# Kernel optimization log

Measured on AMD Instinct MI355X. Metric: run time of the kernel, lower is better.

The kernel has to match this reference:

```python
import jax, jax.numpy as jnp
import numpy as np
import math

B, S, D, H = 4, 2048, 1024, 16
DK = D // H

def setup_inputs() -> dict:
    key = jax.random.key(0)
    ks = jax.random.split(key, 11)
    mk = lambda k, shape: jax.random.normal(k, shape, dtype=jnp.float32)
    inp = {
        'query': mk(ks[0], (B, S, D)),
        'key':   mk(ks[1], (B, S, D)),
        'value': mk(ks[2], (B, S, D)),
        'Wq': mk(ks[3], (D, D)) * 0.02, 'bq': jnp.zeros((D,), jnp.float32),
        'Wk': mk(ks[4], (D, D)) * 0.02, 'bk': jnp.zeros((D,), jnp.float32),
        'Wv': mk(ks[5], (D, D)) * 0.02, 'bv': jnp.zeros((D,), jnp.float32),
        'Wo': mk(ks[6], (D, D)) * 0.02, 'bo': jnp.zeros((D,), jnp.float32),
    }
    return inp

def reference(query, key, value, Wq, bq, Wk, bk, Wv, bv, Wo, bo):
    b, s, d = query.shape
    scale = 1.0 / math.sqrt(DK)
    def proj(x, W, bias):
        # nn.Linear: x @ W.T + b, then split heads -> [b, h, s, dk]
        return (x @ W.T + bias).reshape(b, s, H, DK).transpose(0, 2, 1, 3)
    q = proj(query, Wq, bq)
    k = proj(key, Wk, bk)
    v = proj(value, Wv, bv)
    scores = jnp.einsum('bhqd,bhkd->bhqk', q, k) * scale  # [b,h,s,s]
    attn = jax.nn.softmax(scores, axis=-1)
    # dropout is identity in eval/reference mode
    x = jnp.einsum('bhqk,bhkd->bhqd', attn, v)
    x = x.transpose(0, 2, 1, 3).reshape(b, s, d)
    return x @ Wo.T + bo
```

## Files before the change

kernel.cpp:

```cpp
#include <hip/hip_runtime.h>
#include <stdint.h>

#define DEV static __device__ __forceinline__

typedef __bf16 bf16_t;
typedef bf16_t bf16x8 __attribute__((ext_vector_type(8)));
typedef bf16_t bf16x4 __attribute__((ext_vector_type(4)));
typedef float f32x4 __attribute__((ext_vector_type(4)));

static constexpr int Bc = 4, Sc = 2048, Dc = 1024, Hc = 16, DKc = 64;
static constexpr int Mrows = Bc * Sc;

DEV unsigned short f2bf(float f) {
  unsigned int u = __float_as_uint(f);
  u += 0x7fffu + ((u >> 16) & 1u);
  return (unsigned short)(u >> 16);
}

DEV float fexp2(float x) {
#if __has_builtin(__builtin_amdgcn_exp2f)
  return __builtin_amdgcn_exp2f(x);
#else
  return exp2f(x);
#endif
}

#if __has_builtin(__builtin_amdgcn_mfma_f32_16x16x16_bf16)
DEV f32x4 mfma16(bf16x4 a, bf16x4 b, f32x4 c) {
  return __builtin_amdgcn_mfma_f32_16x16x16_bf16(a, b, c, 0, 0, 0);
}
#elif __has_builtin(__builtin_amdgcn_mfma_f32_16x16x16bf16_1k)
typedef short s16x4 __attribute__((ext_vector_type(4)));
DEV f32x4 mfma16(bf16x4 a, bf16x4 b, f32x4 c) {
  union U { bf16x4 h; s16x4 s; };
  U ua, ub; ua.h = a; ub.h = b;
  return __builtin_amdgcn_mfma_f32_16x16x16bf16_1k(ua.s, ub.s, c, 0, 0, 0);
}
#else
DEV f32x4 mfma16(bf16x4 a, bf16x4 b, f32x4 c) {
  asm("v_mfma_f32_16x16x16_bf16 %0, %1, %2, %0" : "+v"(c) : "v"(a), "v"(b));
  return c;
}
#endif

DEV void gload_lds16(const void* g, void* l) {
  __builtin_amdgcn_global_load_lds(
      (const __attribute__((address_space(1))) void*)g,
      (__attribute__((address_space(3))) void*)l, 16, 0, 0);
}

DEV bf16x8 cvt8(float4 a, float4 b) {
  bf16x8 r;
  r[0] = (bf16_t)a.x; r[1] = (bf16_t)a.y; r[2] = (bf16_t)a.z; r[3] = (bf16_t)a.w;
  r[4] = (bf16_t)b.x; r[5] = (bf16_t)b.y; r[6] = (bf16_t)b.z; r[7] = (bf16_t)b.w;
  return r;
}

__global__ void __launch_bounds__(256) cvt_bf16_seg_kernel(
    const float* __restrict__ s0, const float* __restrict__ s1,
    const float* __restrict__ s2, const float* __restrict__ s3,
    unsigned short* __restrict__ out, int lg) {
  int i = blockIdx.x * blockDim.x + threadIdx.x;
  int seg = i >> lg, j = i & ((1 << lg) - 1);
  const float* src = seg == 0 ? s0 : seg == 1 ? s1 : seg == 2 ? s2 : s3;
  float4 v = reinterpret_cast<const float4*>(src)[j];
  ushort4 o;
  o.x = f2bf(v.x); o.y = f2bf(v.y); o.z = f2bf(v.z); o.w = f2bf(v.w);
  reinterpret_cast<ushort4*>(out)[i] = o;
}

template <bool QKV>
__global__ void __launch_bounds__(256) gemm_dbuf_kernel(
    const void* __restrict__ A0v, const void* __restrict__ A1v,
    const void* __restrict__ A2v,
    const unsigned short* __restrict__ W0, const unsigned short* __restrict__ W1,
    const unsigned short* __restrict__ W2,
    const float* __restrict__ b0, const float* __restrict__ b1,
    const float* __restrict__ b2,
    void* __restrict__ C0, void* __restrict__ C1, void* __restrict__ C2,
    int M, int N, int K, float scale0) {
  __shared__ unsigned short lA[2][128 * 32];
  __shared__ unsigned short lB[2][128 * 32];
  const int t = threadIdx.x;
  const int wv = t >> 6, ln = t & 63;
  const int l15 = ln & 15, lhi = ln >> 4;

  const void* Av; const unsigned short* W;
  const float* bias; void* Cout; float scale; int mode;
  if (QKV) {
    const int z = blockIdx.z;
    Av = z == 0 ? A0v : z == 1 ? A1v : A2v;
    W = z == 0 ? W0 : z == 1 ? W1 : W2;
    bias = z == 0 ? b0 : z == 1 ? b1 : b2;
    Cout = z == 0 ? C0 : z == 1 ? C1 : C2;
    scale = z == 0 ? scale0 : 1.0f;
    mode = z == 2 ? 2 : 1;
  } else {
    Av = A0v; W = W0; bias = b0; Cout = C0; scale = scale0; mode = 0;
  }

  const int nwg = gridDim.x * gridDim.y;
  const int hw = blockIdx.y * gridDim.x + blockIdx.x;
  const int chunk = nwg >> 3;
  const int swzid = (hw & 7) * chunk + (hw >> 3);
  const int m0 = (swzid / gridDim.x) * 128, n0 = (swzid % gridDim.x) * 128;
  const int wr = wv >> 1, wc = wv & 1;
  const int swzR = (l15 & 3) << 4;

  const int rowA = t >> 2;
  const int colS = ((t & 3) ^ (rowA & 3)) * 8;
  const unsigned short* wS = W + (size_t)(n0 + rowA) * K + colS;
  const size_t rstep = (size_t)64 * K;
  const int d0 = t * 16, d1 = 4096 + t * 16;
  const float* aF = QKV ? (const float*)Av + (size_t)(m0 + rowA) * K + colS : nullptr;
  const unsigned short* aB =
      QKV ? nullptr : (const unsigned short*)Av + (size_t)(m0 + rowA) * K + colS;

  f32x4 acc[4][4] = {};

#define WSTAGE(bi, k0_)                                        \
  do {                                                         \
    gload_lds16(wS + (k0_), (char*)lB[bi] + d0);               \
    gload_lds16(wS + rstep + (k0_), (char*)lB[bi] + d1);       \
  } while (0)
#define ABSTAGE(bi, k0_)                                       \
  do {                                                         \
    gload_lds16(aB + (k0_), (char*)lA[bi] + d0);               \
    gload_lds16(aB + rstep + (k0_), (char*)lA[bi] + d1);       \
  } while (0)

  WSTAGE(0, 0);
  if (QKV) {
    float4 a0 = *(const float4*)(aF);
    float4 a1 = *(const float4*)(aF + 4);
    float4 a2 = *(const float4*)(aF + rstep);
    float4 a3 = *(const float4*)(aF + rstep + 4);
    *reinterpret_cast<bf16x8*>((char*)lA[0] + d0) = cvt8(a0, a1);
    *reinterpret_cast<bf16x8*>((char*)lA[0] + d1) = cvt8(a2, a3);
  } else {
    ABSTAGE(0, 0);
  }
  asm volatile("s_waitcnt vmcnt(0) lgkmcnt(0)" ::: "memory");
  __builtin_amdgcn_s_barrier();
  __builtin_amdgcn_sched_barrier(0);

  const int NK = K >> 5;
  for (int tk = 0; tk < NK; ++tk) {
    const int cur = tk & 1, nxt = cur ^ 1;
    float4 a0, a1, a2, a3;
    const bool pre = (tk + 1 < NK);
    if (pre) {
      WSTAGE(nxt, (tk + 1) * 32);
      if (QKV) {
        const float* p = aF + (tk + 1) * 32;
        a0 = *(const float4*)(p);
        a1 = *(const float4*)(p + 4);
        a2 = *(const float4*)(p + rstep);
        a3 = *(const float4*)(p + rstep + 4);
      } else {
        ABSTAGE(nxt, (tk + 1) * 32);
      }
    }

    bf16x8 af[4], bfr[4];
#pragma unroll
    for (int i = 0; i < 4; ++i)
      af[i] = *reinterpret_cast<const bf16x8*>(
          (char*)lA[cur] + (((wr * 64 + i * 16 + l15) * 64 + lhi * 16) ^ swzR));
#pragma unroll
    for (int j = 0; j < 4; ++j)
      bfr[j] = *reinterpret_cast<const bf16x8*>(
          (char*)lB[cur] + (((wc * 64 + j * 16 + l15) * 64 + lhi * 16) ^ swzR));
#pragma unroll
    for (int i = 0; i < 4; ++i)
#pragma unroll
      for (int j = 0; j < 4; ++j)
        acc[i][j] = __builtin_amdgcn_mfma_f32_16x16x32_bf16(af[i], bfr[j], acc[i][j], 0, 0, 0);

    if (QKV && pre) {
      *reinterpret_cast<bf16x8*>((char*)lA[nxt] + d0) = cvt8(a0, a1);
      *reinterpret_cast<bf16x8*>((char*)lA[nxt] + d1) = cvt8(a2, a3);
    }

    asm volatile("s_waitcnt vmcnt(0) lgkmcnt(0)" ::: "memory");
    __builtin_amdgcn_s_barrier();
    __builtin_amdgcn_sched_barrier(0);
  }
#undef WSTAGE
#undef ABSTAGE

#pragma unroll
  for (int i = 0; i < 4; ++i)
#pragma unroll
    for (int j = 0; j < 4; ++j) {
      int n = n0 + wc * 64 + j * 16 + l15;
      float bv = bias[n];
      if (QKV && mode == 2) {
        int mb = m0 + wr * 64 + i * 16 + lhi * 4;
        int sl = mb & (Sc - 1);
        int pl = (sl & ~60) | ((sl & 48) >> 2) | ((sl & 12) << 2);
        ushort4 ov;
        ov.x = f2bf((acc[i][j][0] + bv) * scale);
        ov.y = f2bf((acc[i][j][1] + bv) * scale);
        ov.z = f2bf((acc[i][j][2] + bv) * scale);
        ov.w = f2bf((acc[i][j][3] + bv) * scale);
        *reinterpret_cast<ushort4*>((unsigned short*)Cout +
            ((size_t)(mb >> 11) * Dc + n) * Sc + pl) = ov;
      } else {
#pragma unroll
        for (int jj = 0; jj < 4; ++jj) {
          int m = m0 + wr * 64 + i * 16 + lhi * 4 + jj;
          float v = (acc[i][j][jj] + bv) * scale;
          if (QKV)
            ((unsigned short*)Cout)[(size_t)m * N + n] = f2bf(v);
          else
            ((float*)Cout)[(size_t)m * N + n] = v;
        }
      }
    }
}

__global__ void __launch_bounds__(512, 4) attn_kernel(
    const unsigned short* __restrict__ Q, const unsigned short* __restrict__ Kk,
    const unsigned short* __restrict__ Vt, unsigned short* __restrict__ X) {
  __shared__ unsigned short lK[2][128 * 64];
  __shared__ unsigned short lVT[2][64 * 128];
  const int t = threadIdx.x;
  const int wv = t >> 6, ln = t & 63;
  const int l15 = ln & 15, lhi = ln >> 4;
  const int q0 = blockIdx.x * 128;
  const int h = blockIdx.y, b = blockIdx.z;
  const size_t base = (size_t)b * Sc * Dc;
  const int hoff = h * DKc;

  bf16x8 qf[2];
  {
    const unsigned short* qp = Q + base + (size_t)(q0 + wv * 16 + l15) * Dc + hoff + lhi * 8;
    qf[0] = *reinterpret_cast<const bf16x8*>(qp);
    qf[1] = *reinterpret_cast<const bf16x8*>(qp + 32);
  }

  const int kvr = t >> 3;
  const int kcol = ((t & 7) * 8) ^ ((kvr & 7) << 3);
  const unsigned short* kS = Kk + base + (size_t)kvr * Dc + hoff + kcol;
  const int vdk = t >> 4;
  const int vkv = ((t & 15) * 8) ^ ((vdk & 7) << 3);
  const unsigned short* vS = Vt + ((size_t)b * Dc + hoff + vdk) * Sc + vkv;

  float nm = 0.f;
  f32x4 xacc[4] = {};
  f32x4 lsum = {};
  const int swzK = (l15 & 7) << 4;

  bf16x4 ones4;
#pragma unroll
  for (int i = 0; i < 4; ++i) ones4[i] = (bf16_t)1.0f;

#define DSTAGE(bi, kv0_)                                                        \
  do {                                                                          \
    gload_lds16(kS + (size_t)(kv0_)*Dc, (char*)lK[bi] + t * 16);                \
    gload_lds16(kS + (size_t)((kv0_) + 64) * Dc, (char*)lK[bi] + 8192 + t * 16);\
    gload_lds16(vS + (kv0_), (char*)lVT[bi] + t * 16);                          \
    gload_lds16(vS + (size_t)32 * Sc + (kv0_), (char*)lVT[bi] + 8192 + t * 16); \
  } while (0)

  DSTAGE(0, 0);
  asm volatile("s_waitcnt vmcnt(0)" ::: "memory");
  __builtin_amdgcn_s_barrier();
  __builtin_amdgcn_sched_barrier(0);

  const int NT2 = Sc / 128;
  for (int tt = 0; tt < NT2; ++tt) {
    const int cur = tt & 1;
    if (tt + 1 < NT2) DSTAGE(cur ^ 1, (tt + 1) * 128);

    const char* K_ = (const char*)lK[cur];
    const char* VT_ = (const char*)lVT[cur];

    f32x4 nm4 = {nm, nm, nm, nm};
    f32x4 sacc[2][4];
    __builtin_amdgcn_s_setprio(1);
#pragma unroll
    for (int s64 = 0; s64 < 2; ++s64)
#pragma unroll
      for (int ct = 0; ct < 4; ++ct) {
        f32x4 z = nm4;
#pragma unroll
        for (int kk = 0; kk < 2; ++kk) {
          bf16x8 kf = *reinterpret_cast<const bf16x8*>(
              K_ + (((s64 * 64 + ct * 16 + l15) * 128 + kk * 64 + lhi * 16) ^ swzK));
          z = __builtin_amdgcn_mfma_f32_16x16x32_bf16(kf, qf[kk], z, 0, 0, 0);
        }
        sacc[s64][ct] = z;
      }
    __builtin_amdgcn_s_setprio(0);

    float m0a = fmaxf(fmaxf(sacc[0][0][0], sacc[0][0][1]), fmaxf(sacc[0][0][2], sacc[0][0][3]));
    float m0b = fmaxf(fmaxf(sacc[0][1][0], sacc[0][1][1]), fmaxf(sacc[0][1][2], sacc[0][1][3]));
    float m0c = fmaxf(fmaxf(sacc[0][2][0], sacc[0][2][1]), fmaxf(sacc[0][2][2], sacc[0][2][3]));
    float m0d = fmaxf(fmaxf(sacc[0][3][0], sacc[0][3][1]), fmaxf(sacc[0][3][2], sacc[0][3][3]));
    float m1a = fmaxf(fmaxf(sacc[1][0][0], sacc[1][0][1]), fmaxf(sacc[1][0][2], sacc[1][0][3]));
    float m1b = fmaxf(fmaxf(sacc[1][1][0], sacc[1][1][1]), fmaxf(sacc[1][1][2], sacc[1][1][3]));
    float m1c = fmaxf(fmaxf(sacc[1][2][0], sacc[1][2][1]), fmaxf(sacc[1][2][2], sacc[1][2][3]));
    float m1d = fmaxf(fmaxf(sacc[1][3][0], sacc[1][3][1]), fmaxf(sacc[1][3][2], sacc[1][3][3]));
    float mt = fmaxf(fmaxf(fmaxf(m0a, m0b), fmaxf(m0c, m0d)),
                     fmaxf(fmaxf(m1a, m1b), fmaxf(m1c, m1d)));

    if (__any(mt > 8.0f)) {
      float mtr = fmaxf(mt, __shfl_xor(mt, 16));
      mtr = fmaxf(mtr, __shfl_xor(mtr, 32));
      float mte = fmaxf(mtr, 0.f);
      float corr = fexp2(-mte);
      nm -= mte;
#pragma unroll
      for (int jj = 0; jj < 4; ++jj) {
        float cO = __shfl(corr, lhi * 4 + jj);
        lsum[jj] *= cO;
#pragma unroll
        for (int dt = 0; dt < 4; ++dt) xacc[dt][jj] *= cO;
      }
#pragma unroll
      for (int s64 = 0; s64 < 2; ++s64)
#pragma unroll
        for (int ct = 0; ct < 4; ++ct)
#pragma unroll
          for (int jj = 0; jj < 4; ++jj) sacc[s64][ct][jj] -= mte;
    }

    __builtin_amdgcn_s_setprio(1);
#pragma unroll
    for (int s64 = 0; s64 < 2; ++s64) {
      bf16x4 pa[4];
#pragma unroll
      for (int ct = 0; ct < 4; ++ct)
#pragma unroll
        for (int jj = 0; jj < 4; ++jj)
          pa[ct][jj] = (bf16_t)fexp2(sacc[s64][ct][jj]);
#pragma unroll
      for (int ct = 0; ct < 4; ++ct) lsum = mfma16(pa[ct], ones4, lsum);
#pragma unroll
      for (int dt = 0; dt < 4; ++dt) {
#pragma unroll
        for (int sel = 0; sel < 2; ++sel) {
          bf16x8 vb2 = *reinterpret_cast<const bf16x8*>(
              VT_ + (((dt * 16 + l15) * 256 + s64 * 128 + lhi * 32 + sel * 16) ^ swzK));
          bf16x4 vlo = __builtin_shufflevector(vb2, vb2, 0, 1, 2, 3);
          bf16x4 vhi = __builtin_shufflevector(vb2, vb2, 4, 5, 6, 7);
          xacc[dt] = mfma16(pa[2 * sel + 0], vlo, xacc[dt]);
          xacc[dt] = mfma16(pa[2 * sel + 1], vhi, xacc[dt]);
        }
      }
    }
    __builtin_amdgcn_s_setprio(0);

    asm volatile("s_waitcnt vmcnt(0)" ::: "memory");
    __builtin_amdgcn_s_barrier();
    __builtin_amdgcn_sched_barrier(0);
  }
#undef DSTAGE

  float iO[4];
#pragma unroll
  for (int jj = 0; jj < 4; ++jj) iO[jj] = 1.0f / lsum[jj];

  unsigned short* xp = X + base + (size_t)(q0 + wv * 16) * Dc + hoff;
#pragma unroll
  for (int dt = 0; dt < 4; ++dt)
#pragma unroll
    for (int jj = 0; jj < 4; ++jj) {
      int r = lhi * 4 + jj;
      xp[(size_t)r * Dc + dt * 16 + l15] = f2bf(xacc[dt][jj] * iO[jj]);
    }
}

extern "C" void kernel_launch(void* const* d_in, const int* in_sizes, int n_in,
                              void* d_out, int out_size, void* d_ws, size_t ws_size,
                              hipStream_t stream) {
  const float* query = (const float*)d_in[0];
  const float* key   = (const float*)d_in[1];
  const float* value = (const float*)d_in[2];
  const float* Wq = (const float*)d_in[3];
  const float* bq = (const float*)d_in[4];
  const float* Wk = (const float*)d_in[5];
  const float* bk = (const float*)d_in[6];
  const float* Wv = (const float*)d_in[7];
  const float* bv = (const float*)d_in[8];
  const float* Wo = (const float*)d_in[9];
  const float* bo = (const float*)d_in[10];

  const size_t NBS = (size_t)Mrows * Dc;
  const size_t NW  = (size_t)Dc * Dc;
  unsigned short* bWq  = (unsigned short*)d_ws;
  unsigned short* bWk  = bWq + NW;
  unsigned short* bWv  = bWk + NW;
  unsigned short* bWo  = bWv + NW;
  unsigned short* Qp   = bWo + NW;
  unsigned short* Kp   = Qp + NBS;
  unsigned short* Vtp  = Kp + NBS;
  unsigned short* Xp   = Vtp + NBS;

  cvt_bf16_seg_kernel<<<(int)(4 * NW / 1024), 256, 0, stream>>>(
      Wq, Wk, Wv, Wo, bWq, 18);

  gemm_dbuf_kernel<true><<<dim3(Dc / 128, Mrows / 128, 3), 256, 0, stream>>>(
      query, key, value, bWq, bWk, bWv, bq, bk, bv, Qp, Kp, Vtp,
      Mrows, Dc, Dc, 0.125f * 1.44269504088896340736f);

  attn_kernel<<<dim3(Sc / 128, Hc, Bc), 512, 0, stream>>>(Qp, Kp, Vtp, Xp);

  gemm_dbuf_kernel<false><<<dim3(Dc / 128, Mrows / 128, 1), 256, 0, stream>>>(
      Xp, nullptr, nullptr, bWo, nullptr, nullptr, bo, nullptr, nullptr,
      d_out, nullptr, nullptr, Mrows, Dc, Dc, 1.0f);
}
```

Baseline: 226.1 us.

## Triple-buffer GEMM LDS tiles with two-stage-ahead prefetch and partial waitcnt

Moves the projection GEMM kernel from double to triple buffering in LDS. Loads are issued two K-steps ahead, and the full vmcnt(0) drain each iteration becomes a partial wait, so global loads stay in flight across MFMA work. The fp32-input QKV path keeps a second register set of prefetched A values to convert and write one step later. The cost is 50% more LDS per block, which may lower occupancy, and more registers in the QKV path. The hand-counted vmcnt values must match the actual number of outstanding loads to stay correct.

```diff
diff --git a/kernel.cpp b/kernel.cpp
--- a/kernel.cpp
+++ b/kernel.cpp
@@ -79,8 +79,8 @@
     const float* __restrict__ b2,
     void* __restrict__ C0, void* __restrict__ C1, void* __restrict__ C2,
     int M, int N, int K, float scale0) {
-  __shared__ unsigned short lA[2][128 * 32];
-  __shared__ unsigned short lB[2][128 * 32];
+  __shared__ unsigned short lA[3][128 * 32];
+  __shared__ unsigned short lB[3][128 * 32];
   const int t = threadIdx.x;
   const int wv = t >> 6, ln = t & 63;
   const int l15 = ln & 15, lhi = ln >> 4;
@@ -117,77 +117,105 @@
       QKV ? nullptr : (const unsigned short*)Av + (size_t)(m0 + rowA) * K + colS;
 
   f32x4 acc[4][4] = {};
-
-#define WSTAGE(bi, k0_)                                        \
+  const int NK = K >> 5;
+
+#define WST(bi, k0_)                                           \
   do {                                                         \
     gload_lds16(wS + (k0_), (char*)lB[bi] + d0);               \
     gload_lds16(wS + rstep + (k0_), (char*)lB[bi] + d1);       \
   } while (0)
-#define ABSTAGE(bi, k0_)                                       \
+
+#define MFMA_BLOCK(cur_)                                                        \
+  do {                                                                          \
+    bf16x8 af[4], bfr[4];                                                       \
+    _Pragma("unroll") for (int i = 0; i < 4; ++i)                               \
+      af[i] = *reinterpret_cast<const bf16x8*>(                                 \
+          (char*)lA[cur_] + (((wr * 64 + i * 16 + l15) * 64 + lhi * 16) ^ swzR));\
+    _Pragma("unroll") for (int j = 0; j < 4; ++j)                               \
+      bfr[j] = *reinterpret_cast<const bf16x8*>(                                \
+          (char*)lB[cur_] + (((wc * 64 + j * 16 + l15) * 64 + lhi * 16) ^ swzR));\
+    _Pragma("unroll") for (int i = 0; i < 4; ++i)                               \
+      _Pragma("unroll") for (int j = 0; j < 4; ++j)                             \
+        acc[i][j] = __builtin_amdgcn_mfma_f32_16x16x32_bf16(af[i], bfr[j],      \
+                                                            acc[i][j], 0, 0, 0);\
+  } while (0)
+
+  if (QKV) {
+    float4 a0, a1, a2, a3;
+    float4 n0_, n1_, n2_, n3_;
+#define ALD(k0_)                                               \
+  do {                                                         \
+    const float* p = aF + (k0_);                               \
+    a0 = *(const float4*)(p);     a1 = *(const float4*)(p + 4);\
+    a2 = *(const float4*)(p + rstep); a3 = *(const float4*)(p + rstep + 4);\
+  } while (0)
+#define ALDN(k0_)                                              \
+  do {                                                         \
+    const float* p = aF + (k0_);                               \
+    n0_ = *(const float4*)(p);     n1_ = *(const float4*)(p + 4);\
+    n2_ = *(const float4*)(p + rstep); n3_ = *(const float4*)(p + rstep + 4);\
+  } while (0)
+#define AWR(bi)                                                \
+  do {                                                         \
+    *reinterpret_cast<bf16x8*>((char*)lA[bi] + d0) = cvt8(a0, a1);\
+    *reinterpret_cast<bf16x8*>((char*)lA[bi] + d1) = cvt8(a2, a3);\
+  } while (0)
+    WST(0, 0);
+    ALD(0);
+    AWR(0);
+    WST(1, 32);
+    ALD(32);
+    asm volatile("s_waitcnt vmcnt(6) lgkmcnt(0)" ::: "memory");
+    __builtin_amdgcn_s_barrier();
+    __builtin_amdgcn_sched_barrier(0);
+
+    for (int tk = 0; tk < NK; ++tk) {
+      const int cur = tk % 3;
+      const bool hn = (tk + 1 < NK), hn2 = (tk + 2 < NK);
+      if (hn2) {
+        WST((tk + 2) % 3, (tk + 2) * 32);
+        ALDN((tk + 2) * 32);
+      }
+      __builtin_amdgcn_sched_barrier(0);
+      MFMA_BLOCK(cur);
+      if (hn) AWR((tk + 1) % 3);
+      if (hn2) { a0 = n0_; a1 = n1_; a2 = n2_; a3 = n3_; }
+      if (hn2)
+        asm volatile("s_waitcnt vmcnt(6) lgkmcnt(0)" ::: "memory");
+      else
+        asm volatile("s_waitcnt vmcnt(0) lgkmcnt(0)" ::: "memory");
+      __builtin_amdgcn_s_barrier();
+      __builtin_amdgcn_sched_barrier(0);
+    }
+#undef ALD
+#undef ALDN
+#undef AWR
+  } else {
+#define AST(bi, k0_)                                           \
   do {                                                         \
     gload_lds16(aB + (k0_), (char*)lA[bi] + d0);               \
     gload_lds16(aB + rstep + (k0_), (char*)lA[bi] + d1);       \
   } while (0)
-
-  WSTAGE(0, 0);
-  if (QKV) {
-    float4 a0 = *(const float4*)(aF);
-    float4 a1 = *(const float4*)(aF + 4);
-    float4 a2 = *(const float4*)(aF + rstep);
-    float4 a3 = *(const float4*)(aF + rstep + 4);
-    *reinterpret_cast<bf16x8*>((char*)lA[0] + d0) = cvt8(a0, a1);
-    *reinterpret_cast<bf16x8*>((char*)lA[0] + d1) = cvt8(a2, a3);
-  } else {
-    ABSTAGE(0, 0);
+    AST(0, 0); WST(0, 0);
+    AST(1, 32); WST(1, 32);
+    for (int tk = 0; tk < NK; ++tk) {
+      const int cur = tk % 3;
+      if (tk == NK - 1)
+        asm volatile("s_waitcnt vmcnt(0)" ::: "memory");
+      else
+        asm volatile("s_waitcnt vmcnt(4)" ::: "memory");
+      __builtin_amdgcn_s_barrier();
+      __builtin_amdgcn_sched_barrier(0);
+      if (tk + 2 < NK) {
+        AST((tk + 2) % 3, (tk + 2) * 32);
+        WST((tk + 2) % 3, (tk + 2) * 32);
+      }
+      MFMA_BLOCK(cur);
+    }
+#undef AST
   }
-  asm volatile("s_waitcnt vmcnt(0) lgkmcnt(0)" ::: "memory");
-  __builtin_amdgcn_s_barrier();
-  __builtin_amdgcn_sched_barrier(0);
-
-  const int NK = K >> 5;
-  for (int tk = 0; tk < NK; ++tk) {
-    const int cur = tk & 1, nxt = cur ^ 1;
-    float4 a0, a1, a2, a3;
-    const bool pre = (tk + 1 < NK);
-    if (pre) {
-      WSTAGE(nxt, (tk + 1) * 32);
-      if (QKV) {
-        const float* p = aF + (tk + 1) * 32;
-        a0 = *(const float4*)(p);
-        a1 = *(const float4*)(p + 4);
-        a2 = *(const float4*)(p + rstep);
-        a3 = *(const float4*)(p + rstep + 4);
-      } else {
-        ABSTAGE(nxt, (tk + 1) * 32);
-      }
-    }
-
-    bf16x8 af[4], bfr[4];
-#pragma unroll
-    for (int i = 0; i < 4; ++i)
-      af[i] = *reinterpret_cast<const bf16x8*>(
-          (char*)lA[cur] + (((wr * 64 + i * 16 + l15) * 64 + lhi * 16) ^ swzR));
-#pragma unroll
-    for (int j = 0; j < 4; ++j)
-      bfr[j] = *reinterpret_cast<const bf16x8*>(
-          (char*)lB[cur] + (((wc * 64 + j * 16 + l15) * 64 + lhi * 16) ^ swzR));
-#pragma unroll
-    for (int i = 0; i < 4; ++i)
-#pragma unroll
-      for (int j = 0; j < 4; ++j)
-        acc[i][j] = __builtin_amdgcn_mfma_f32_16x16x32_bf16(af[i], bfr[j], acc[i][j], 0, 0, 0);
-
-    if (QKV && pre) {
-      *reinterpret_cast<bf16x8*>((char*)lA[nxt] + d0) = cvt8(a0, a1);
-      *reinterpret_cast<bf16x8*>((char*)lA[nxt] + d1) = cvt8(a2, a3);
-    }
-
-    asm volatile("s_waitcnt vmcnt(0) lgkmcnt(0)" ::: "memory");
-    __builtin_amdgcn_s_barrier();
-    __builtin_amdgcn_sched_barrier(0);
-  }
-#undef WSTAGE
-#undef ABSTAGE
+#undef WST
+#undef MFMA_BLOCK
 
 #pragma unroll
   for (int i = 0; i < 4; ++i)
```

Result: faster. 220.1 us (-2.7%).
